# Kernel tuning notes

Hardware: AMD Instinct MI355X
Metric: run time of the kernel (lower is better)

The kernel has to match this reference:

```python
import jax, jax.numpy as jnp
import numpy as np

N = 20000
E = 640000
C_IN = 256
C_OUT = 256
K = 2
EPS = 1e-12


def setup_inputs() -> dict:
    key = jax.random.key(0)
    k1, k2, k3, k4, k5 = jax.random.split(key, 5)
    x = jax.random.normal(k1, (N, C_IN), dtype=jnp.float32)
    edge_index = jax.random.randint(k2, (2, E), 0, N, dtype=jnp.int64)
    edge_weights = jax.random.uniform(k3, (E,), dtype=jnp.float32)
    lin_w = jax.random.normal(k4, (C_OUT, C_IN), dtype=jnp.float32) / np.sqrt(C_IN)
    lin_b = jax.random.normal(k5, (C_OUT,), dtype=jnp.float32) * 0.01
    return {"x": x, "edge_index": edge_index, "edge_weights": edge_weights,
            "lin_w": lin_w, "lin_b": lin_b}


def reference(x, edge_index, edge_weights, lin_w, lin_b):
    row, col = edge_index[0], edge_index[1]  # source -> target

    # F.normalize(x, p=2, dim=-1)
    nrm = jnp.sqrt(jnp.sum(x * x, axis=-1, keepdims=True))
    x = x / jnp.maximum(nrm, EPS)

    # gcn_norm with add_self_loops=False (PyG): deg over target nodes
    deg = jax.ops.segment_sum(edge_weights, col, num_segments=N)
    deg_inv_sqrt = jnp.where(deg > 0, 1.0 / jnp.sqrt(deg), 0.0)
    norm = deg_inv_sqrt[row] * edge_weights * deg_inv_sqrt[col]  # [E]

    # K-hop propagation: out[col] += norm * x[row]
    for _ in range(K):
        msgs = norm[:, None] * x[row]                     # [E, C]
        x = jax.ops.segment_sum(msgs, col, num_segments=N)

    # Linear layer of SGConv
    return x @ lin_w.T + lin_b
```

## Files before the change

### kernel.cpp

```cpp
#include <hip/hip_runtime.h>
#include <hip/hip_bf16.h>

#define N_NODES 20000
#define N_EDGES 640000
#define C 256
#define S 96
#define CNTS 16

#define SCATTER_BLOCKS 2500
#define NORM_BLOCKS 10000
#define WCONV_BLOCKS 256

typedef __attribute__((ext_vector_type(8))) short short8;
typedef __attribute__((ext_vector_type(4))) float float4v;
typedef __attribute__((ext_vector_type(4))) unsigned uint4v;

__device__ inline unsigned short f2bf(float f) {
    unsigned u = __float_as_uint(f);
    unsigned r = (u + 0x7fffu + ((u >> 16) & 1u)) >> 16;
    return (unsigned short)r;
}
__device__ inline float bf_lo(unsigned u) { return __uint_as_float(u << 16); }
__device__ inline float bf_hi(unsigned u) { return __uint_as_float(u & 0xffff0000u); }
__device__ inline float bf_hi_raw(unsigned u) { return __uint_as_float(u); }

__global__ __launch_bounds__(256) void fused_pre_kernel(
        const int* __restrict__ ei, const float* __restrict__ w,
        const float* __restrict__ x, const float* __restrict__ lw,
        int* __restrict__ cnt, unsigned* __restrict__ csr,
        unsigned* __restrict__ xs32, unsigned short* __restrict__ Wb) {
    int b = blockIdx.x;
    int t = threadIdx.x;
    if (b < SCATTER_BLOCKS) {
        __shared__ int okw[4];
        unsigned long long m = __ballot(ei[2 * t + 1] == 0);
        if ((t & 63) == 0) okw[t >> 6] = (m == 0xFFFFFFFFFFFFFFFFull) ? 1 : 0;
        __syncthreads();
        int flag = okw[0] & okw[1] & okw[2] & okw[3];
        int e = b * 256 + t;
        int r, c;
        if (flag) { r = ei[2 * e]; c = ei[2 * (N_EDGES + e)]; }
        else      { r = ei[e];     c = ei[N_EDGES + e]; }
        int pos = atomicAdd(&cnt[c * CNTS], 1);
        if (pos < S) csr[c * S + pos] = (unsigned)r | ((unsigned)f2bf(w[e]) << 16);
    } else if (b < SCATTER_BLOCKS + NORM_BLOCKS) {
        int half = t >> 7;
        int tt = t & 127;
        int i = (b - SCATTER_BLOCKS) * 2 + half;
        float2 v = ((const float2*)x)[(size_t)i * 128 + tt];
        float ss = v.x * v.x + v.y * v.y;
        #pragma unroll
        for (int o = 32; o > 0; o >>= 1) ss += __shfl_down(ss, o, 64);
        __shared__ float wsum[4];
        if ((t & 63) == 0) wsum[t >> 6] = ss;
        __syncthreads();
        float tot = wsum[half * 2] + wsum[half * 2 + 1];
        float inv = 1.0f / fmaxf(sqrtf(tot), 1e-12f);
        xs32[(size_t)i * 128 + tt] =
            (unsigned)f2bf(v.x * inv) | ((unsigned)f2bf(v.y * inv) << 16);
    } else {
        int idx = (b - SCATTER_BLOCKS - NORM_BLOCKS) * 256 + t;
        Wb[idx] = f2bf(lw[idx]);
    }
}

__global__ void deg_dis_kernel(const unsigned* __restrict__ csr, const int* __restrict__ cnt,
                               float* __restrict__ dis, unsigned char* __restrict__ ncap) {
    int wv = threadIdx.x >> 6;
    int lane = threadIdx.x & 63;
    int i = blockIdx.x * 4 + wv;
    int n = cnt[i * CNTS];
    if (n > S) n = S;
    float s = 0.0f;
    if (lane < n) s = bf_hi(__builtin_nontemporal_load(&csr[i * S + lane]));
    if (lane + 64 < n) s += bf_hi(__builtin_nontemporal_load(&csr[i * S + lane + 64]));
    #pragma unroll
    for (int o = 32; o > 0; o >>= 1) s += __shfl_down(s, o, 64);
    if (lane == 0) {
        dis[i] = (s > 0.0f) ? rsqrtf(s) : 0.0f;
        ncap[i] = (unsigned char)n;
    }
}

template <int POW, int SRC_DIS>
__global__ __launch_bounds__(256) void gather_kernel(const unsigned char* __restrict__ ncap,
                                                     const unsigned* __restrict__ csr,
                                                     const float* __restrict__ dis,
                                                     const unsigned* __restrict__ in,
                                                     unsigned* __restrict__ out) {
    __shared__ uint2 st_all[4][S];
    int wvi = threadIdx.x >> 6;
    int lane = threadIdx.x & 63;
    int i = blockIdx.x * 4 + wvi;
    int n = ncap[i];
    int nup = (n + 7) & ~7;
    uint2* st = st_all[wvi];
    if (lane < n) {
        unsigned p = __builtin_nontemporal_load(&csr[i * S + lane]);
        unsigned s = p & 0xffffu;
        float wv = bf_hi(p);
        if (SRC_DIS) wv *= dis[s];
        st[lane] = make_uint2(s << 9, __float_as_uint(wv));
    }
    if (lane + 64 < n) {
        unsigned p = __builtin_nontemporal_load(&csr[i * S + lane + 64]);
        unsigned s = p & 0xffffu;
        float wv = bf_hi(p);
        if (SRC_DIS) wv *= dis[s];
        st[lane + 64] = make_uint2(s << 9, __float_as_uint(wv));
    }
    {
        int k = n + lane;
        if (k < nup) st[k] = make_uint2(0u, 0u);
    }
    __builtin_amdgcn_wave_barrier();

    int grp = lane >> 5;
    unsigned hb = (unsigned)(lane & 31) << 4;
    const char* base = (const char*)in;
    float2 c0 = {0.f, 0.f}, c1 = {0.f, 0.f}, c2 = {0.f, 0.f}, c3 = {0.f, 0.f};
    for (int j = 0; j < nup; j += 8) {
        uint2 e0 = st[j + grp];
        uint2 e1 = st[j + 2 + grp];
        uint2 e2 = st[j + 4 + grp];
        uint2 e3 = st[j + 6 + grp];
        uint4v v0 = *(const uint4v*)(base + (e0.x + hb));
        uint4v v1 = *(const uint4v*)(base + (e1.x + hb));
        uint4v v2 = *(const uint4v*)(base + (e2.x + hb));
        uint4v v3 = *(const uint4v*)(base + (e3.x + hb));
        float w0 = __uint_as_float(e0.y), w1 = __uint_as_float(e1.y);
        float w2 = __uint_as_float(e2.y), w3 = __uint_as_float(e3.y);
        c0.x += w0 * bf_lo(v0.x); c0.y += w0 * bf_hi_raw(v0.x);
        c1.x += w0 * bf_lo(v0.y); c1.y += w0 * bf_hi_raw(v0.y);
        c2.x += w0 * bf_lo(v0.z); c2.y += w0 * bf_hi_raw(v0.z);
        c3.x += w0 * bf_lo(v0.w); c3.y += w0 * bf_hi_raw(v0.w);
        c0.x += w1 * bf_lo(v1.x); c0.y += w1 * bf_hi_raw(v1.x);
        c1.x += w1 * bf_lo(v1.y); c1.y += w1 * bf_hi_raw(v1.y);
        c2.x += w1 * bf_lo(v1.z); c2.y += w1 * bf_hi_raw(v1.z);
        c3.x += w1 * bf_lo(v1.w); c3.y += w1 * bf_hi_raw(v1.w);
        c0.x += w2 * bf_lo(v2.x); c0.y += w2 * bf_hi_raw(v2.x);
        c1.x += w2 * bf_lo(v2.y); c1.y += w2 * bf_hi_raw(v2.y);
        c2.x += w2 * bf_lo(v2.z); c2.y += w2 * bf_hi_raw(v2.z);
        c3.x += w2 * bf_lo(v2.w); c3.y += w2 * bf_hi_raw(v2.w);
        c0.x += w3 * bf_lo(v3.x); c0.y += w3 * bf_hi_raw(v3.x);
        c1.x += w3 * bf_lo(v3.y); c1.y += w3 * bf_hi_raw(v3.y);
        c2.x += w3 * bf_lo(v3.z); c2.y += w3 * bf_hi_raw(v3.z);
        c3.x += w3 * bf_lo(v3.w); c3.y += w3 * bf_hi_raw(v3.w);
    }
    c0.x += __shfl_down(c0.x, 32, 64); c0.y += __shfl_down(c0.y, 32, 64);
    c1.x += __shfl_down(c1.x, 32, 64); c1.y += __shfl_down(c1.y, 32, 64);
    c2.x += __shfl_down(c2.x, 32, 64); c2.y += __shfl_down(c2.y, 32, 64);
    c3.x += __shfl_down(c3.x, 32, 64); c3.y += __shfl_down(c3.y, 32, 64);
    if (lane < 32) {
        float d = dis[i];
        float sc = (POW == 2) ? d * d : d;
        uint4v r;
        r.x = (unsigned)f2bf(c0.x * sc) | ((unsigned)f2bf(c0.y * sc) << 16);
        r.y = (unsigned)f2bf(c1.x * sc) | ((unsigned)f2bf(c1.y * sc) << 16);
        r.z = (unsigned)f2bf(c2.x * sc) | ((unsigned)f2bf(c2.y * sc) << 16);
        r.w = (unsigned)f2bf(c3.x * sc) | ((unsigned)f2bf(c3.y * sc) << 16);
        __builtin_nontemporal_store(r, (uint4v*)(out + (size_t)i * 128) + lane);
    }
}

__global__ __launch_bounds__(256, 4) void gemm_kernel(const unsigned short* __restrict__ h,
                                                      const unsigned short* __restrict__ Wb,
                                                      const float* __restrict__ b,
                                                      float* __restrict__ out) {
    int wv = threadIdx.x >> 6;
    int lane = threadIdx.x & 63;
    int m = lane & 15;
    int q = lane >> 4;
    int rg = blockIdx.x >> 2;
    int cg = blockIdx.x & 3;
    int rowbase = rg * 64 + wv * 16;
    int rowA = rowbase + m;
    if (rowA > N_NODES - 1) rowA = N_NODES - 1;
    float4v acc[4];
    #pragma unroll
    for (int nt = 0; nt < 4; nt++) acc[nt] = (float4v){0.f, 0.f, 0.f, 0.f};
    #pragma unroll
    for (int kt = 0; kt < 8; kt++) {
        int kb = kt * 32 + q * 8;
        short8 a = *(const short8*)(h + (size_t)rowA * C + kb);
        #pragma unroll
        for (int nt = 0; nt < 4; nt++) {
            int col = cg * 64 + nt * 16 + m;
            short8 bb = *(const short8*)(Wb + (size_t)col * C + kb);
            acc[nt] = __builtin_amdgcn_mfma_f32_16x16x32_bf16(a, bb, acc[nt], 0, 0, 0);
        }
    }
    #pragma unroll
    for (int nt = 0; nt < 4; nt++) {
        int col = cg * 64 + nt * 16 + m;
        float bias = b[col];
        #pragma unroll
        for (int r = 0; r < 4; r++) {
            int ro = rowbase + q * 4 + r;
            if (ro < N_NODES)
                __builtin_nontemporal_store(acc[nt][r] + bias, &out[(size_t)ro * C + col]);
        }
    }
}

extern "C" void kernel_launch(void* const* d_in, const int* in_sizes, int n_in,
                              void* d_out, int out_size, void* d_ws, size_t ws_size,
                              hipStream_t stream) {
    const float* x  = (const float*)d_in[0];
    const int*   ei = (const int*)d_in[1];
    const float* w  = (const float*)d_in[2];
    const float* lw = (const float*)d_in[3];
    const float* lb = (const float*)d_in[4];
    float* out = (float*)d_out;

    char* ws = (char*)d_ws;
    size_t off = 0;
    auto alloc = [&](size_t bytes) -> void* {
        void* p = ws + off;
        off = (off + bytes + 255) & ~(size_t)255;
        return p;
    };
    unsigned* bufA   = (unsigned*)alloc((size_t)N_NODES * 128 * 4);
    unsigned* bufB   = (unsigned*)alloc((size_t)N_NODES * 128 * 4);
    float* dis       = (float*)alloc((size_t)N_NODES * 4);
    int*   cnt       = (int*)alloc((size_t)N_NODES * CNTS * 4);
    unsigned* csr    = (unsigned*)alloc((size_t)N_NODES * S * 4);
    unsigned short* Wb = (unsigned short*)alloc((size_t)C * C * 2);
    unsigned char* ncap = (unsigned char*)alloc((size_t)N_NODES);
    (void)ws_size; (void)in_sizes; (void)n_in; (void)out_size;

    (void)hipMemsetAsync(cnt, 0, (size_t)N_NODES * CNTS * 4, stream);

    fused_pre_kernel<<<SCATTER_BLOCKS + NORM_BLOCKS + WCONV_BLOCKS, 256, 0, stream>>>(
        ei, w, x, lw, cnt, csr, bufA, Wb);
    deg_dis_kernel<<<N_NODES / 4, 256, 0, stream>>>(csr, cnt, dis, ncap);
    gather_kernel<2, 1><<<N_NODES / 4, 256, 0, stream>>>(ncap, csr, dis, bufA, bufB);
    gather_kernel<1, 0><<<N_NODES / 4, 256, 0, stream>>>(ncap, csr, dis, bufB, bufA);
    gemm_kernel<<<313 * 4, 256, 0, stream>>>(
        (const unsigned short*)bufA, Wb, lb, out);
}
```

Baseline: 207.4 us.

## Fold source degree scaling into normalized features and stage GEMM weights in LDS

The row L2-normalization is split out of the fused pre-kernel into its own kernel that runs after the degree computation, so each node's features are also scaled by its deg^-1/2. This removes the per-edge random dis[src] lookup in the first gather, leaving only a bit-mask of the packed CSR weight. The GEMM now copies its 64-column slice of the bf16 weights into padded shared memory once per block, replacing repeated global loads of B. The trade-offs are an extra kernel launch, less overlap between normalization and scatter, and an added block barrier in the GEMM.

```diff
diff --git a/kernel.cpp b/kernel.cpp
--- a/kernel.cpp
+++ b/kernel.cpp
@@ -8,8 +8,10 @@
 #define CNTS 16
 
 #define SCATTER_BLOCKS 2500
+#define WCONV_BLOCKS 256
 #define NORM_BLOCKS 10000
-#define WCONV_BLOCKS 256
+
+#define BPAD 264
 
 typedef __attribute__((ext_vector_type(8))) short short8;
 typedef __attribute__((ext_vector_type(4))) float float4v;
@@ -24,11 +26,11 @@
 __device__ inline float bf_hi(unsigned u) { return __uint_as_float(u & 0xffff0000u); }
 __device__ inline float bf_hi_raw(unsigned u) { return __uint_as_float(u); }
 
-__global__ __launch_bounds__(256) void fused_pre_kernel(
+__global__ __launch_bounds__(256) void scatter_kernel(
         const int* __restrict__ ei, const float* __restrict__ w,
-        const float* __restrict__ x, const float* __restrict__ lw,
+        const float* __restrict__ lw,
         int* __restrict__ cnt, unsigned* __restrict__ csr,
-        unsigned* __restrict__ xs32, unsigned short* __restrict__ Wb) {
+        unsigned short* __restrict__ Wb) {
     int b = blockIdx.x;
     int t = threadIdx.x;
     if (b < SCATTER_BLOCKS) {
@@ -43,23 +45,8 @@
         else      { r = ei[e];     c = ei[N_EDGES + e]; }
         int pos = atomicAdd(&cnt[c * CNTS], 1);
         if (pos < S) csr[c * S + pos] = (unsigned)r | ((unsigned)f2bf(w[e]) << 16);
-    } else if (b < SCATTER_BLOCKS + NORM_BLOCKS) {
-        int half = t >> 7;
-        int tt = t & 127;
-        int i = (b - SCATTER_BLOCKS) * 2 + half;
-        float2 v = ((const float2*)x)[(size_t)i * 128 + tt];
-        float ss = v.x * v.x + v.y * v.y;
-        #pragma unroll
-        for (int o = 32; o > 0; o >>= 1) ss += __shfl_down(ss, o, 64);
-        __shared__ float wsum[4];
-        if ((t & 63) == 0) wsum[t >> 6] = ss;
-        __syncthreads();
-        float tot = wsum[half * 2] + wsum[half * 2 + 1];
-        float inv = 1.0f / fmaxf(sqrtf(tot), 1e-12f);
-        xs32[(size_t)i * 128 + tt] =
-            (unsigned)f2bf(v.x * inv) | ((unsigned)f2bf(v.y * inv) << 16);
     } else {
-        int idx = (b - SCATTER_BLOCKS - NORM_BLOCKS) * 256 + t;
+        int idx = (b - SCATTER_BLOCKS) * 256 + t;
         Wb[idx] = f2bf(lw[idx]);
     }
 }
@@ -82,7 +69,27 @@
     }
 }
 
-template <int POW, int SRC_DIS>
+__global__ __launch_bounds__(256) void norm_kernel(
+        const float* __restrict__ x, const float* __restrict__ dis,
+        unsigned* __restrict__ xs32) {
+    int t = threadIdx.x;
+    int half = t >> 7;
+    int tt = t & 127;
+    int i = blockIdx.x * 2 + half;
+    float2 v = ((const float2*)x)[(size_t)i * 128 + tt];
+    float ss = v.x * v.x + v.y * v.y;
+    #pragma unroll
+    for (int o = 32; o > 0; o >>= 1) ss += __shfl_down(ss, o, 64);
+    __shared__ float wsum[4];
+    if ((t & 63) == 0) wsum[t >> 6] = ss;
+    __syncthreads();
+    float tot = wsum[half * 2] + wsum[half * 2 + 1];
+    float inv = dis[i] / fmaxf(sqrtf(tot), 1e-12f);
+    xs32[(size_t)i * 128 + tt] =
+        (unsigned)f2bf(v.x * inv) | ((unsigned)f2bf(v.y * inv) << 16);
+}
+
+template <int POW>
 __global__ __launch_bounds__(256) void gather_kernel(const unsigned char* __restrict__ ncap,
                                                      const unsigned* __restrict__ csr,
                                                      const float* __restrict__ dis,
@@ -97,17 +104,11 @@
     uint2* st = st_all[wvi];
     if (lane < n) {
         unsigned p = __builtin_nontemporal_load(&csr[i * S + lane]);
-        unsigned s = p & 0xffffu;
-        float wv = bf_hi(p);
-        if (SRC_DIS) wv *= dis[s];
-        st[lane] = make_uint2(s << 9, __float_as_uint(wv));
+        st[lane] = make_uint2((p & 0xffffu) << 9, p & 0xffff0000u);
     }
     if (lane + 64 < n) {
         unsigned p = __builtin_nontemporal_load(&csr[i * S + lane + 64]);
-        unsigned s = p & 0xffffu;
-        float wv = bf_hi(p);
-        if (SRC_DIS) wv *= dis[s];
-        st[lane + 64] = make_uint2(s << 9, __float_as_uint(wv));
+        st[lane + 64] = make_uint2((p & 0xffffu) << 9, p & 0xffff0000u);
     }
     {
         int k = n + lane;
@@ -167,12 +168,24 @@
                                                       const unsigned short* __restrict__ Wb,
                                                       const float* __restrict__ b,
                                                       float* __restrict__ out) {
-    int wv = threadIdx.x >> 6;
-    int lane = threadIdx.x & 63;
+    __shared__ unsigned short Bs[64 * BPAD];
+    int t = threadIdx.x;
+    int wv = t >> 6;
+    int lane = t & 63;
     int m = lane & 15;
     int q = lane >> 4;
     int rg = blockIdx.x >> 2;
     int cg = blockIdx.x & 3;
+    #pragma unroll
+    for (int it = 0; it < 8; it++) {
+        int ch = it * 256 + t;
+        int col = ch >> 5;
+        int off8 = (ch & 31) * 8;
+        *(uint4v*)(Bs + col * BPAD + off8) =
+            *(const uint4v*)(Wb + (size_t)(cg * 64 + col) * C + off8);
+    }
+    __syncthreads();
+
     int rowbase = rg * 64 + wv * 16;
     int rowA = rowbase + m;
     if (rowA > N_NODES - 1) rowA = N_NODES - 1;
@@ -185,8 +198,7 @@
         short8 a = *(const short8*)(h + (size_t)rowA * C + kb);
         #pragma unroll
         for (int nt = 0; nt < 4; nt++) {
-            int col = cg * 64 + nt * 16 + m;
-            short8 bb = *(const short8*)(Wb + (size_t)col * C + kb);
+            short8 bb = *(const short8*)(Bs + (nt * 16 + m) * BPAD + kb);
             acc[nt] = __builtin_amdgcn_mfma_f32_16x16x32_bf16(a, bb, acc[nt], 0, 0, 0);
         }
     }
@@ -231,11 +243,12 @@
 
     (void)hipMemsetAsync(cnt, 0, (size_t)N_NODES * CNTS * 4, stream);
 
-    fused_pre_kernel<<<SCATTER_BLOCKS + NORM_BLOCKS + WCONV_BLOCKS, 256, 0, stream>>>(
-        ei, w, x, lw, cnt, csr, bufA, Wb);
+    scatter_kernel<<<SCATTER_BLOCKS + WCONV_BLOCKS, 256, 0, stream>>>(
+        ei, w, lw, cnt, csr, Wb);
     deg_dis_kernel<<<N_NODES / 4, 256, 0, stream>>>(csr, cnt, dis, ncap);
-    gather_kernel<2, 1><<<N_NODES / 4, 256, 0, stream>>>(ncap, csr, dis, bufA, bufB);
-    gather_kernel<1, 0><<<N_NODES / 4, 256, 0, stream>>>(ncap, csr, dis, bufB, bufA);
+    norm_kernel<<<NORM_BLOCKS, 256, 0, stream>>>(x, dis, bufA);
+    gather_kernel<2><<<N_NODES / 4, 256, 0, stream>>>(ncap, csr, dis, bufA, bufB);
+    gather_kernel<1><<<N_NODES / 4, 256, 0, stream>>>(ncap, csr, dis, bufB, bufA);
     gemm_kernel<<<313 * 4, 256, 0, stream>>>(
         (const unsigned short*)bufA, Wb, lb, out);
 }
```

Result: faster. 200.0 us (-3.6%).
